# Performance work log

Hardware: AMD Instinct MI355X
Metric: run time of the kernel (lower is better)

## Reference

```python
import jax, jax.numpy as jnp
import numpy as np

EPS = 1e-5


def _binary_act(x):
    # Forward: sign(x). Backward: piecewise-polynomial surrogate (ApproxSign STE).
    out3 = jnp.where(x < -1, -1.0,
            jnp.where(x < 0, x * x + 2.0 * x,
             jnp.where(x < 1, -x * x + 2.0 * x, 1.0)))
    return jax.lax.stop_gradient(jnp.sign(x) - out3) + out3


def _binarize_weights(w):
    # Per-output-channel scaling factor (detached), forward = scale*sign(w),
    # backward flows through clamp(w, -1, 1) (STE).
    scale = jax.lax.stop_gradient(jnp.mean(jnp.abs(w), axis=(1, 2, 3), keepdims=True))
    clipped = jnp.clip(w, -1.0, 1.0)
    return jax.lax.stop_gradient(scale * jnp.sign(w) - clipped) + clipped


def setup_inputs() -> dict:
    key = jax.random.key(0)
    kx, kw = jax.random.split(key)
    B, Cin, Cout, H, W = 32, 128, 128, 56, 56
    x = jax.random.normal(kx, (B, Cin, H, W), dtype=jnp.float32)
    # HardBinaryConv: weight = rand(n)*0.001 permuted then reshaped -> just random in [0, 0.001)
    w = jax.random.uniform(kw, (Cout, Cin, 3, 3), dtype=jnp.float32) * 0.001
    return {
        "x": x,
        "bias0": jnp.zeros((Cin,), jnp.float32),   # move0 LearnableBias
        "w": w,                                     # HardBinaryConv latent weights
        "gamma": jnp.ones((Cout,), jnp.float32),    # BN weight
        "beta": jnp.zeros((Cout,), jnp.float32),    # BN bias
        "bias1": jnp.zeros((Cout,), jnp.float32),   # move1
        "alpha": jnp.full((Cout,), 0.25, jnp.float32),  # PReLU per-channel
        "bias2": jnp.zeros((Cout,), jnp.float32),   # move2
    }


def reference(x, bias0, w, gamma, beta, bias1, alpha, bias2):
    def pc(v):  # per-channel broadcast (1, C, 1, 1)
        return v[None, :, None, None]

    residual = x
    out = x + pc(bias0)                     # move0
    out = _binary_act(out)                  # binary activation
    bw = _binarize_weights(w)               # {-scale, +scale} weights
    y = jax.lax.conv_general_dilated(
        out, bw, window_strides=(1, 1), padding=((1, 1), (1, 1)),
        dimension_numbers=("NCHW", "OIHW", "NCHW"))
    # BatchNorm2d (training mode: biased batch statistics over N,H,W)
    mean = jnp.mean(y, axis=(0, 2, 3), keepdims=True)
    var = jnp.mean(jnp.square(y - mean), axis=(0, 2, 3), keepdims=True)
    y = (y - mean) * jax.lax.rsqrt(var + EPS) * pc(gamma) + pc(beta)
    y = y + residual
    y = y + pc(bias1)                       # move1
    y = jnp.where(y >= 0, y, pc(alpha) * y)  # PReLU
    y = y + pc(bias2)                       # move2
    return y
```

## Files before the change

### kernel.cpp

```cpp
#include <hip/hip_runtime.h>
#include <stdint.h>

#define NB 32
#define NC 128
#define NH 56
#define NW 56
#define NHW_ (NH * NW)
#define NPIX (NB * NHW_)
#define NO 128
#define NK 1152
#define NRP 28
#define NSLOT (NB * NRP)

#define PADH 58
#define PADW 66
#define PAD_BYTES ((size_t)NB * PADH * PADW * 2 * 8)

typedef unsigned long long u64;

__device__ __forceinline__ int wave_sum_dpp(int v) {
    v += __builtin_amdgcn_update_dpp(0, v, 0x111, 0xF, 0xF, true);
    v += __builtin_amdgcn_update_dpp(0, v, 0x112, 0xF, 0xF, true);
    v += __builtin_amdgcn_update_dpp(0, v, 0x114, 0xF, 0xF, true);
    v += __builtin_amdgcn_update_dpp(0, v, 0x118, 0xF, 0xF, true);
    v += __builtin_amdgcn_update_dpp(0, v, 0x142, 0xF, 0xF, true);
    v += __builtin_amdgcn_update_dpp(0, v, 0x143, 0xF, 0xF, true);
    return v;
}

__global__ __launch_bounds__(256) void pack_act(const float* __restrict__ x,
                                                const float* __restrict__ bias0,
                                                u64* __restrict__ packAp) {
    int p = blockIdx.x * 256 + threadIdx.x;
    if (p >= NPIX) return;
    int n = p / NHW_;
    int rem = p - n * NHW_;
    int h = rem / NW, wcol = rem - h * NW;
    const float* xb = x + (size_t)n * NC * NHW_ + rem;
    u64 w0 = 0, w1 = 0;
#pragma unroll 8
    for (int c = 0; c < 64; ++c)
        w0 |= (u64)((xb[(size_t)c * NHW_] + bias0[c]) > 0.f) << c;
#pragma unroll 8
    for (int c = 0; c < 64; ++c)
        w1 |= (u64)((xb[(size_t)(c + 64) * NHW_] + bias0[c + 64]) > 0.f) << c;
    size_t idx = (((size_t)n * PADH + (h + 1)) * PADW + (wcol + 1)) * 2;
    packAp[idx]     = w0;
    packAp[idx + 1] = w1;
}

__global__ __launch_bounds__(64) void pack_wgt(const float* __restrict__ w,
                                               u64* __restrict__ packWT,
                                               float* __restrict__ scaleW,
                                               int* __restrict__ corrW) {
    __shared__ u64 sb[18];
    int o = blockIdx.x;
    int t = threadIdx.x;
    const float* wo = w + (size_t)o * NK;
    float s = 0.f;
    for (int i = t; i < NK; i += 64) s += fabsf(wo[i]);
    for (int off = 32; off; off >>= 1) s += __shfl_down(s, off);
    if (t == 0) scaleW[o] = s / (float)NK;
    if (t < 18) {
        int tap = t >> 1;
        int j   = t & 1;
        u64 bits = 0;
        for (int cc = 0; cc < 64; ++cc) {
            int c = j * 64 + cc;
            bits |= (u64)(wo[c * 9 + tap] > 0.f) << cc;
        }
        packWT[((size_t)tap * NO + o) * 2 + j] = bits;
        sb[t] = bits;
    }
    __syncthreads();
    if (t == 0) {
        int cv[9];
#pragma unroll
        for (int tap = 0; tap < 9; ++tap)
            cv[tap] = NC - 2 * (__popcll(sb[2 * tap]) + __popcll(sb[2 * tap + 1]));
        int* cw = corrW + o * 8;
        cw[0] = cv[0] + cv[3] + cv[6];
        cw[1] = cv[2] + cv[5] + cv[8];
        cw[2] = cv[0] + cv[1] + cv[2];
        cw[3] = cv[6] + cv[7] + cv[8];
        cw[4] = cv[0];
        cw[5] = cv[2];
        cw[6] = cv[6];
        cw[7] = cv[8];
    }
}

template <int MODE>
__global__ __launch_bounds__(256) void conv_bin(
    const u64* __restrict__ packAp, const u64* __restrict__ packWT,
    const int* __restrict__ corrW, short* __restrict__ yI,
    int* __restrict__ sumP, int* __restrict__ sqP,
    const float* __restrict__ coefA, const float* __restrict__ coefB,
    const float* __restrict__ alpha, const float* __restrict__ bias2,
    const float* __restrict__ x, float* __restrict__ out) {
    __shared__ u64 lsA[4 * PADW * 2];

    int bid = blockIdx.x;
    int n = bid / (NRP * 2);
    int rem = bid - n * (NRP * 2);
    int hp = rem >> 1;
    int cg = rem & 1;
    int h0 = hp * 2;

    {
        const u64* src = packAp + ((size_t)n * PADH + h0) * PADW * 2;
        for (int i = threadIdx.x; i < 4 * PADW; i += 256) {
            ulonglong2 q = *reinterpret_cast<const ulonglong2*>(src + (size_t)i * 2);
            lsA[i * 2]     = q.x;
            lsA[i * 2 + 1] = q.y;
        }
    }
    __syncthreads();

    int wv = threadIdx.x >> 6, lane = threadIdx.x & 63;
    bool act = lane < NW;
    int obase = __builtin_amdgcn_readfirstlane(cg * 64 + (wv << 4));
    const int* cbase = corrW + obase * 8;
    const u64* lrow = lsA + (size_t)lane * 2;

    int pc0[16], pc1[16];
#pragma unroll
    for (int i = 0; i < 16; ++i) { pc0[i] = 0; pc1[i] = 0; }

#pragma unroll 1
    for (int t = 0; t < 9; ++t) {
        int kh = (t * 11) >> 5;
        int kw = t - kh * 3;
        const u64* wt = packWT + ((size_t)t * NO + obase) * 2;
        int aoff = (kh * PADW + kw) * 2;
        u64 A00 = lrow[aoff],            A01 = lrow[aoff + 1];
        u64 A10 = lrow[aoff + PADW * 2], A11 = lrow[aoff + PADW * 2 + 1];
#pragma unroll
        for (int ch = 0; ch < 16; ++ch) {
            u64 w0 = wt[2 * ch], w1 = wt[2 * ch + 1];
            pc0[ch] += __popcll(A00 ^ w0) + __popcll(A01 ^ w1);
            pc1[ch] += __popcll(A10 ^ w0) + __popcll(A11 ^ w1);
        }
    }

    bool top = (hp == 0), bot = (hp == NRP - 1);
    bool isL = (lane == 0), isR = (lane == NW - 1);
    int sl = n * NRP + hp;
    size_t pixoff = (size_t)n * NO * NHW_ + (size_t)h0 * NW + lane;

#pragma unroll
    for (int ch = 0; ch < 16; ++ch) {
        int o = obase + ch;
        const int* cw = cbase + ch * 8;
        int corrcol = isL ? cw[0] : (isR ? cw[1] : 0);
        int base = NK - corrcol;
        int d0 = base - 2 * pc0[ch];
        int d1 = base - 2 * pc1[ch];
        if (top) d0 -= cw[2] - (isL ? cw[4] : (isR ? cw[5] : 0));
        if (bot) d1 -= cw[3] - (isL ? cw[6] : (isR ? cw[7] : 0));

        if (MODE == 0 && act) {
            short* yp = yI + pixoff + (size_t)o * NHW_;
            yp[0]  = (short)d0;
            yp[NW] = (short)d1;
        }
        if (MODE <= 1) {
            int s = wave_sum_dpp(act ? (d0 + d1) : 0);
            int q = wave_sum_dpp(act ? (__mul24(d0, d0) + __mul24(d1, d1)) : 0);
            if (lane == 63) {
                sumP[o * NSLOT + sl] = s;
                sqP[o * NSLOT + sl]  = q;
            }
        }
        if (MODE == 2 && act) {
            float ca = coefA[o], cb = coefB[o], al = alpha[o], b2 = bias2[o];
            size_t idx = pixoff + (size_t)o * NHW_;
            float t0 = fmaf(ca, (float)d0, cb) + x[idx];
            float t1 = fmaf(ca, (float)d1, cb) + x[idx + NW];
            t0 = t0 >= 0.f ? t0 : al * t0;
            t1 = t1 >= 0.f ? t1 : al * t1;
            out[idx]      = t0 + b2;
            out[idx + NW] = t1 + b2;
        }
    }
}

__global__ __launch_bounds__(64) void bn_coef2(const int* __restrict__ sumP,
                                               const int* __restrict__ sqP,
                                               const float* __restrict__ scaleW,
                                               const float* __restrict__ gamma,
                                               const float* __restrict__ beta,
                                               const float* __restrict__ bias1,
                                               float* __restrict__ coefA,
                                               float* __restrict__ coefB) {
    int o = blockIdx.x;
    int t = threadIdx.x;
    long long s = 0, q = 0;
    for (int i = t; i < NSLOT; i += 64) {
        s += sumP[o * NSLOT + i];
        q += sqP[o * NSLOT + i];
    }
#pragma unroll
    for (int off = 32; off; off >>= 1) {
        s += __shfl_down(s, off);
        q += __shfl_down(q, off);
    }
    if (t == 0) {
        double cnt = (double)NPIX;
        double mean = (double)s / cnt;
        double var = (double)q / cnt - mean * mean;
        if (var < 0.0) var = 0.0;
        float sc = scaleW[o];
        float rs = rsqrtf((float)((double)sc * (double)sc * var) + 1e-5f);
        float g = gamma[o];
        coefA[o] = sc * g * rs;
        coefB[o] = beta[o] - (float)((double)sc * mean) * g * rs + bias1[o];
    }
}

__global__ __launch_bounds__(256) void final_store(const short* __restrict__ yI,
                                                   const float* __restrict__ x,
                                                   const float* __restrict__ coefA,
                                                   const float* __restrict__ coefB,
                                                   const float* __restrict__ alpha,
                                                   const float* __restrict__ bias2,
                                                   float* __restrict__ out) {
    const size_t ngroups = (size_t)NB * NO * NHW_ / 8;
    for (size_t g = (size_t)blockIdx.x * blockDim.x + threadIdx.x; g < ngroups;
         g += (size_t)gridDim.x * blockDim.x) {
        size_t i = g * 8;
        int o = (int)((i / NHW_) % NO);
        float a = coefA[o], bb = coefB[o], al = alpha[o], b2 = bias2[o];
        int4 yv = *reinterpret_cast<const int4*>(yI + i);
        float4 x0 = *reinterpret_cast<const float4*>(x + i);
        float4 x1 = *reinterpret_cast<const float4*>(x + i + 4);
        int q[4] = {yv.x, yv.y, yv.z, yv.w};
        float xs[8] = {x0.x, x0.y, x0.z, x0.w, x1.x, x1.y, x1.z, x1.w};
        float r[8];
#pragma unroll
        for (int j = 0; j < 4; ++j) {
            float lo = (float)(short)(q[j] & 0xffff);
            float hi = (float)(q[j] >> 16);
            float t0 = fmaf(a, lo, bb) + xs[2 * j];
            float t1 = fmaf(a, hi, bb) + xs[2 * j + 1];
            t0 = t0 >= 0.f ? t0 : al * t0;
            t1 = t1 >= 0.f ? t1 : al * t1;
            r[2 * j]     = t0 + b2;
            r[2 * j + 1] = t1 + b2;
        }
        float4 o0 = {r[0], r[1], r[2], r[3]};
        float4 o1 = {r[4], r[5], r[6], r[7]};
        *reinterpret_cast<float4*>(out + i)     = o0;
        *reinterpret_cast<float4*>(out + i + 4) = o1;
    }
}

extern "C" void kernel_launch(void* const* d_in, const int* in_sizes, int n_in,
                              void* d_out, int out_size, void* d_ws, size_t ws_size,
                              hipStream_t stream) {
    (void)in_sizes; (void)n_in; (void)out_size;
    const float* x     = (const float*)d_in[0];
    const float* bias0 = (const float*)d_in[1];
    const float* w     = (const float*)d_in[2];
    const float* gamma = (const float*)d_in[3];
    const float* beta  = (const float*)d_in[4];
    const float* bias1 = (const float*)d_in[5];
    const float* alpha = (const float*)d_in[6];
    const float* bias2 = (const float*)d_in[7];
    float* out = (float*)d_out;
    char* ws = (char*)d_ws;

    u64*   packAp = (u64*)ws;
    u64*   packWT = (u64*)(ws + 1959936);
    int*   corrW  = (int*)(ws + 1978368);
    float* scaleW = (float*)(ws + 1982464);
    float* coefA  = (float*)(ws + 1982976);
    float* coefB  = (float*)(ws + 1983488);
    int*   sumP   = (int*)(ws + 1984000);
    int*   sqP    = (int*)(ws + 2442752);
    short* yI     = (short*)(ws + 2901504);
    bool store = ws_size >= (size_t)2901504 + (size_t)NB * NO * NHW_ * 2;

    hipMemsetAsync(packAp, 0, PAD_BYTES, stream);
    pack_act<<<NPIX / 256, 256, 0, stream>>>(x, bias0, packAp);
    pack_wgt<<<NO, 64, 0, stream>>>(w, packWT, scaleW, corrW);

    if (store) {
        conv_bin<0><<<NB * NRP * 2, 256, 0, stream>>>(
            packAp, packWT, corrW, yI, sumP, sqP,
            nullptr, nullptr, nullptr, nullptr, nullptr, nullptr);
        bn_coef2<<<NO, 64, 0, stream>>>(sumP, sqP, scaleW, gamma, beta, bias1, coefA, coefB);
        final_store<<<2048, 256, 0, stream>>>(yI, x, coefA, coefB, alpha, bias2, out);
    } else {
        conv_bin<1><<<NB * NRP * 2, 256, 0, stream>>>(
            packAp, packWT, corrW, nullptr, sumP, sqP,
            nullptr, nullptr, nullptr, nullptr, nullptr, nullptr);
        bn_coef2<<<NO, 64, 0, stream>>>(sumP, sqP, scaleW, gamma, beta, bias1, coefA, coefB);
        conv_bin<2><<<NB * NRP * 2, 256, 0, stream>>>(
            packAp, packWT, corrW, nullptr, sumP, sqP,
            coefA, coefB, alpha, bias2, x, out);
    }
}
```

Before: 102.2 us.

## Replace XNOR-popcount binary conv with int8 MFMA implicit GEMM, recompute conv

Activations and weights are now packed as ±1 int8 values in NHWC with zero padding. The convolution runs as an implicit GEMM on 32x32x32 int8 MFMA instructions, reading from a swizzled LDS tile of six padded rows. Zero-padding the activations removes the old border-correction terms. The int16 intermediate buffer and final_store pass are dropped in favour of running the conv twice, once for the BN statistics and once fused with the epilogue, which trades double compute for less memory traffic. The int8 activation buffer is 8x larger than the bit-packed one, so packing and the memset move more bytes.

```diff
diff --git a/kernel.cpp b/kernel.cpp
--- a/kernel.cpp
+++ b/kernel.cpp
@@ -2,185 +2,203 @@
 #include <stdint.h>
 
 #define NB 32
-#define NC 128
+#define NCH 128
 #define NH 56
 #define NW 56
-#define NHW_ (NH * NW)
-#define NPIX (NB * NHW_)
-#define NO 128
-#define NK 1152
-#define NRP 28
-#define NSLOT (NB * NRP)
-
-#define PADH 58
-#define PADW 66
-#define PAD_BYTES ((size_t)NB * PADH * PADW * 2 * 8)
-
-typedef unsigned long long u64;
-
-__device__ __forceinline__ int wave_sum_dpp(int v) {
+#define NHW_ 3136
+#define NPIX 100352
+#define PADD 58
+#define IMG_BYTES ((size_t)PADD * PADD * NCH)
+#define ACT_BYTES ((size_t)NB * IMG_BYTES)
+#define NTILE 25
+#define NSLOT (NB * NTILE)
+
+typedef int v4i __attribute__((ext_vector_type(4)));
+typedef int v16i __attribute__((ext_vector_type(16)));
+
+__device__ __forceinline__ int sum32(int v) {
     v += __builtin_amdgcn_update_dpp(0, v, 0x111, 0xF, 0xF, true);
     v += __builtin_amdgcn_update_dpp(0, v, 0x112, 0xF, 0xF, true);
     v += __builtin_amdgcn_update_dpp(0, v, 0x114, 0xF, 0xF, true);
     v += __builtin_amdgcn_update_dpp(0, v, 0x118, 0xF, 0xF, true);
     v += __builtin_amdgcn_update_dpp(0, v, 0x142, 0xF, 0xF, true);
-    v += __builtin_amdgcn_update_dpp(0, v, 0x143, 0xF, 0xF, true);
     return v;
 }
 
-__global__ __launch_bounds__(256) void pack_act(const float* __restrict__ x,
-                                                const float* __restrict__ bias0,
-                                                u64* __restrict__ packAp) {
+__global__ __launch_bounds__(256) void pack_act8(const float* __restrict__ x,
+                                                 const float* __restrict__ bias0,
+                                                 char* __restrict__ act8) {
     int p = blockIdx.x * 256 + threadIdx.x;
     if (p >= NPIX) return;
     int n = p / NHW_;
     int rem = p - n * NHW_;
-    int h = rem / NW, wcol = rem - h * NW;
-    const float* xb = x + (size_t)n * NC * NHW_ + rem;
-    u64 w0 = 0, w1 = 0;
-#pragma unroll 8
-    for (int c = 0; c < 64; ++c)
-        w0 |= (u64)((xb[(size_t)c * NHW_] + bias0[c]) > 0.f) << c;
-#pragma unroll 8
-    for (int c = 0; c < 64; ++c)
-        w1 |= (u64)((xb[(size_t)(c + 64) * NHW_] + bias0[c + 64]) > 0.f) << c;
-    size_t idx = (((size_t)n * PADH + (h + 1)) * PADW + (wcol + 1)) * 2;
-    packAp[idx]     = w0;
-    packAp[idx + 1] = w1;
-}
-
-__global__ __launch_bounds__(64) void pack_wgt(const float* __restrict__ w,
-                                               u64* __restrict__ packWT,
-                                               float* __restrict__ scaleW,
-                                               int* __restrict__ corrW) {
-    __shared__ u64 sb[18];
-    int o = blockIdx.x;
-    int t = threadIdx.x;
-    const float* wo = w + (size_t)o * NK;
+    int h = rem / NW, wc = rem - (rem / NW) * NW;
+    const float* xb = x + (size_t)n * NCH * NHW_ + rem;
+    char* dst = act8 + (size_t)n * IMG_BYTES + ((size_t)(h + 1) * PADD + (wc + 1)) * NCH;
+#pragma unroll
+    for (int g = 0; g < 8; ++g) {
+        int d[4];
+#pragma unroll
+        for (int dw = 0; dw < 4; ++dw) {
+            unsigned v = 0;
+#pragma unroll
+            for (int b = 0; b < 4; ++b) {
+                int c = g * 16 + dw * 4 + b;
+                bool pos = (xb[(size_t)c * NHW_] + bias0[c]) > 0.f;
+                v |= (unsigned)(pos ? 0x01u : 0xFFu) << (8 * b);
+            }
+            d[dw] = (int)v;
+        }
+        v4i q = {d[0], d[1], d[2], d[3]};
+        *reinterpret_cast<v4i*>(dst + g * 16) = q;
+    }
+}
+
+__global__ __launch_bounds__(128) void pack_wgt8(const float* __restrict__ w,
+                                                 char* __restrict__ w8,
+                                                 float* __restrict__ scaleW) {
+    __shared__ float red[128];
+    int o = blockIdx.x, c = threadIdx.x;
+    const float* wo = w + ((size_t)o * NCH + c) * 9;
     float s = 0.f;
-    for (int i = t; i < NK; i += 64) s += fabsf(wo[i]);
-    for (int off = 32; off; off >>= 1) s += __shfl_down(s, off);
-    if (t == 0) scaleW[o] = s / (float)NK;
-    if (t < 18) {
-        int tap = t >> 1;
-        int j   = t & 1;
-        u64 bits = 0;
-        for (int cc = 0; cc < 64; ++cc) {
-            int c = j * 64 + cc;
-            bits |= (u64)(wo[c * 9 + tap] > 0.f) << cc;
-        }
-        packWT[((size_t)tap * NO + o) * 2 + j] = bits;
-        sb[t] = bits;
-    }
+#pragma unroll
+    for (int t = 0; t < 9; ++t) {
+        float v = wo[t];
+        s += fabsf(v);
+        w8[(size_t)t * NCH * NCH + (size_t)o * NCH + c] = (v > 0.f) ? 1 : -1;
+    }
+    red[c] = s;
     __syncthreads();
-    if (t == 0) {
-        int cv[9];
-#pragma unroll
-        for (int tap = 0; tap < 9; ++tap)
-            cv[tap] = NC - 2 * (__popcll(sb[2 * tap]) + __popcll(sb[2 * tap + 1]));
-        int* cw = corrW + o * 8;
-        cw[0] = cv[0] + cv[3] + cv[6];
-        cw[1] = cv[2] + cv[5] + cv[8];
-        cw[2] = cv[0] + cv[1] + cv[2];
-        cw[3] = cv[6] + cv[7] + cv[8];
-        cw[4] = cv[0];
-        cw[5] = cv[2];
-        cw[6] = cv[6];
-        cw[7] = cv[8];
-    }
+    for (int st = 64; st; st >>= 1) {
+        if (c < st) red[c] += red[c + st];
+        __syncthreads();
+    }
+    if (c == 0) scaleW[o] = red[0] / 1152.0f;
 }
 
 template <int MODE>
-__global__ __launch_bounds__(256) void conv_bin(
-    const u64* __restrict__ packAp, const u64* __restrict__ packWT,
-    const int* __restrict__ corrW, short* __restrict__ yI,
+__global__ __launch_bounds__(256) void conv_mfma(
+    const char* __restrict__ act8, const char* __restrict__ w8,
     int* __restrict__ sumP, int* __restrict__ sqP,
     const float* __restrict__ coefA, const float* __restrict__ coefB,
     const float* __restrict__ alpha, const float* __restrict__ bias2,
     const float* __restrict__ x, float* __restrict__ out) {
-    __shared__ u64 lsA[4 * PADW * 2];
+    __shared__ char lds[6 * PADD * NCH];
 
     int bid = blockIdx.x;
-    int n = bid / (NRP * 2);
-    int rem = bid - n * (NRP * 2);
-    int hp = rem >> 1;
-    int cg = rem & 1;
-    int h0 = hp * 2;
-
-    {
-        const u64* src = packAp + ((size_t)n * PADH + h0) * PADW * 2;
-        for (int i = threadIdx.x; i < 4 * PADW; i += 256) {
-            ulonglong2 q = *reinterpret_cast<const ulonglong2*>(src + (size_t)i * 2);
-            lsA[i * 2]     = q.x;
-            lsA[i * 2 + 1] = q.y;
+    int n = bid / NTILE, bt = bid - n * NTILE;
+    int pbase = bt * 128;
+    int h0 = pbase / NW;
+    bool v23 = (pbase + 64) < NHW_;
+
+    const char* an = act8 + (size_t)n * IMG_BYTES;
+    for (int r = 0; r < 6; ++r) {
+        int rp = h0 + r;
+        if (rp > 57) rp = 57;
+        const char* src = an + (size_t)rp * PADD * NCH;
+        char* drow = lds + (size_t)r * PADD * NCH;
+        for (int j = threadIdx.x; j < PADD * 8; j += 256) {
+            int col = j >> 3, g = j & 7;
+            v4i v = *reinterpret_cast<const v4i*>(src + col * NCH + g * 16);
+            *reinterpret_cast<v4i*>(drow + col * NCH + ((g ^ (col & 7)) << 4)) = v;
         }
     }
     __syncthreads();
 
     int wv = threadIdx.x >> 6, lane = threadIdx.x & 63;
-    bool act = lane < NW;
-    int obase = __builtin_amdgcn_readfirstlane(cg * 64 + (wv << 4));
-    const int* cbase = corrW + obase * 8;
-    const u64* lrow = lsA + (size_t)lane * 2;
-
-    int pc0[16], pc1[16];
-#pragma unroll
-    for (int i = 0; i < 16; ++i) { pc0[i] = 0; pc1[i] = 0; }
-
-#pragma unroll 1
-    for (int t = 0; t < 9; ++t) {
-        int kh = (t * 11) >> 5;
-        int kw = t - kh * 3;
-        const u64* wt = packWT + ((size_t)t * NO + obase) * 2;
-        int aoff = (kh * PADW + kw) * 2;
-        u64 A00 = lrow[aoff],            A01 = lrow[aoff + 1];
-        u64 A10 = lrow[aoff + PADW * 2], A11 = lrow[aoff + PADW * 2 + 1];
-#pragma unroll
-        for (int ch = 0; ch < 16; ++ch) {
-            u64 w0 = wt[2 * ch], w1 = wt[2 * ch + 1];
-            pc0[ch] += __popcll(A00 ^ w0) + __popcll(A01 ^ w1);
-            pc1[ch] += __popcll(A10 ^ w0) + __popcll(A11 ^ w1);
-        }
-    }
-
-    bool top = (hp == 0), bot = (hp == NRP - 1);
-    bool isL = (lane == 0), isR = (lane == NW - 1);
-    int sl = n * NRP + hp;
-    size_t pixoff = (size_t)n * NO * NHW_ + (size_t)h0 * NW + lane;
-
-#pragma unroll
-    for (int ch = 0; ch < 16; ++ch) {
-        int o = obase + ch;
-        const int* cw = cbase + ch * 8;
-        int corrcol = isL ? cw[0] : (isR ? cw[1] : 0);
-        int base = NK - corrcol;
-        int d0 = base - 2 * pc0[ch];
-        int d1 = base - 2 * pc1[ch];
-        if (top) d0 -= cw[2] - (isL ? cw[4] : (isR ? cw[5] : 0));
-        if (bot) d1 -= cw[3] - (isL ? cw[6] : (isR ? cw[7] : 0));
-
-        if (MODE == 0 && act) {
-            short* yp = yI + pixoff + (size_t)o * NHW_;
-            yp[0]  = (short)d0;
-            yp[NW] = (short)d1;
-        }
-        if (MODE <= 1) {
-            int s = wave_sum_dpp(act ? (d0 + d1) : 0);
-            int q = wave_sum_dpp(act ? (__mul24(d0, d0) + __mul24(d1, d1)) : 0);
-            if (lane == 63) {
-                sumP[o * NSLOT + sl] = s;
-                sqP[o * NSLOT + sl]  = q;
-            }
-        }
-        if (MODE == 2 && act) {
-            float ca = coefA[o], cb = coefB[o], al = alpha[o], b2 = bias2[o];
-            size_t idx = pixoff + (size_t)o * NHW_;
-            float t0 = fmaf(ca, (float)d0, cb) + x[idx];
-            float t1 = fmaf(ca, (float)d1, cb) + x[idx + NW];
+    int l31 = lane & 31, hl = lane >> 5;
+    int og = wv;
+
+    int p0 = pbase + l31;
+    int ph0 = p0 / NW, pw0 = p0 - ph0 * NW;
+    int p1 = p0 + 32, ph1 = p1 / NW, pw1 = p1 - ph1 * NW;
+    int p2 = p0 + 64, ph2 = p2 / NW, pw2 = p2 - ph2 * NW;
+    int p3 = p0 + 96, ph3 = p3 / NW, pw3 = p3 - ph3 * NW;
+    int rb0 = (ph0 - h0) * (PADD * NCH);
+    int rb1 = (ph1 - h0) * (PADD * NCH);
+    int rb2 = (ph2 - h0) * (PADD * NCH);
+    int rb3 = (ph3 - h0) * (PADD * NCH);
+
+    const char* wlane = w8 + ((size_t)(og * 32 + l31)) * NCH + hl * 16;
+
+    v16i acc0 = {0}, acc1 = {0}, acc2 = {0}, acc3 = {0};
+
+#pragma unroll
+    for (int tap = 0; tap < 9; ++tap) {
+        const int th = tap / 3, tw = tap - 3 * (tap / 3);
+#pragma unroll
+        for (int ks = 0; ks < 4; ++ks) {
+            v4i a = *reinterpret_cast<const v4i*>(wlane + tap * (NCH * NCH) + ks * 32);
+            int gq = ks * 2 + hl;
+            {
+                int col = pw0 + tw;
+                int off = rb0 + th * (PADD * NCH) + col * NCH + ((gq ^ (col & 7)) << 4);
+                v4i b = *reinterpret_cast<const v4i*>(lds + off);
+                acc0 = __builtin_amdgcn_mfma_i32_32x32x32_i8(a, b, acc0, 0, 0, 0);
+            }
+            {
+                int col = pw1 + tw;
+                int off = rb1 + th * (PADD * NCH) + col * NCH + ((gq ^ (col & 7)) << 4);
+                v4i b = *reinterpret_cast<const v4i*>(lds + off);
+                acc1 = __builtin_amdgcn_mfma_i32_32x32x32_i8(a, b, acc1, 0, 0, 0);
+            }
+            if (v23) {
+                {
+                    int col = pw2 + tw;
+                    int off = rb2 + th * (PADD * NCH) + col * NCH + ((gq ^ (col & 7)) << 4);
+                    v4i b = *reinterpret_cast<const v4i*>(lds + off);
+                    acc2 = __builtin_amdgcn_mfma_i32_32x32x32_i8(a, b, acc2, 0, 0, 0);
+                }
+                {
+                    int col = pw3 + tw;
+                    int off = rb3 + th * (PADD * NCH) + col * NCH + ((gq ^ (col & 7)) << 4);
+                    v4i b = *reinterpret_cast<const v4i*>(lds + off);
+                    acc3 = __builtin_amdgcn_mfma_i32_32x32x32_i8(a, b, acc3, 0, 0, 0);
+                }
+            }
+        }
+    }
+
+    if (MODE == 0) {
+        int slot = n * NTILE + bt;
+#pragma unroll
+        for (int r = 0; r < 16; ++r) {
+            int d0 = acc0[r], d1 = acc1[r];
+            int s = d0 + d1;
+            int q = d0 * d0 + d1 * d1;
+            if (v23) {
+                int d2 = acc2[r], d3 = acc3[r];
+                s += d2 + d3;
+                q += d2 * d2 + d3 * d3;
+            }
+            s = sum32(s);
+            q = sum32(q);
+            if (l31 == 31) {
+                int ch = og * 32 + (r & 3) + 8 * (r >> 2) + 4 * hl;
+                sumP[ch * NSLOT + slot] = s;
+                sqP[ch * NSLOT + slot] = q;
+            }
+        }
+    } else {
+#pragma unroll
+        for (int r = 0; r < 16; ++r) {
+            int ch = og * 32 + (r & 3) + 8 * (r >> 2) + 4 * hl;
+            float ca = coefA[ch], cb = coefB[ch], al = alpha[ch], b2 = bias2[ch];
+            size_t base = ((size_t)n * NCH + ch) * NHW_ + pbase + l31;
+            float t0 = fmaf(ca, (float)acc0[r], cb) + x[base];
             t0 = t0 >= 0.f ? t0 : al * t0;
+            out[base] = t0 + b2;
+            float t1 = fmaf(ca, (float)acc1[r], cb) + x[base + 32];
             t1 = t1 >= 0.f ? t1 : al * t1;
-            out[idx]      = t0 + b2;
-            out[idx + NW] = t1 + b2;
+            out[base + 32] = t1 + b2;
+            if (v23) {
+                float t2 = fmaf(ca, (float)acc2[r], cb) + x[base + 64];
+                t2 = t2 >= 0.f ? t2 : al * t2;
+                out[base + 64] = t2 + b2;
+                float t3 = fmaf(ca, (float)acc3[r], cb) + x[base + 96];
+                t3 = t3 >= 0.f ? t3 : al * t3;
+                out[base + 96] = t3 + b2;
+            }
         }
     }
 }
@@ -218,47 +236,10 @@
     }
 }
 
-__global__ __launch_bounds__(256) void final_store(const short* __restrict__ yI,
-                                                   const float* __restrict__ x,
-                                                   const float* __restrict__ coefA,
-                                                   const float* __restrict__ coefB,
-                                                   const float* __restrict__ alpha,
-                                                   const float* __restrict__ bias2,
-                                                   float* __restrict__ out) {
-    const size_t ngroups = (size_t)NB * NO * NHW_ / 8;
-    for (size_t g = (size_t)blockIdx.x * blockDim.x + threadIdx.x; g < ngroups;
-         g += (size_t)gridDim.x * blockDim.x) {
-        size_t i = g * 8;
-        int o = (int)((i / NHW_) % NO);
-        float a = coefA[o], bb = coefB[o], al = alpha[o], b2 = bias2[o];
-        int4 yv = *reinterpret_cast<const int4*>(yI + i);
-        float4 x0 = *reinterpret_cast<const float4*>(x + i);
-        float4 x1 = *reinterpret_cast<const float4*>(x + i + 4);
-        int q[4] = {yv.x, yv.y, yv.z, yv.w};
-        float xs[8] = {x0.x, x0.y, x0.z, x0.w, x1.x, x1.y, x1.z, x1.w};
-        float r[8];
-#pragma unroll
-        for (int j = 0; j < 4; ++j) {
-            float lo = (float)(short)(q[j] & 0xffff);
-            float hi = (float)(q[j] >> 16);
-            float t0 = fmaf(a, lo, bb) + xs[2 * j];
-            float t1 = fmaf(a, hi, bb) + xs[2 * j + 1];
-            t0 = t0 >= 0.f ? t0 : al * t0;
-            t1 = t1 >= 0.f ? t1 : al * t1;
-            r[2 * j]     = t0 + b2;
-            r[2 * j + 1] = t1 + b2;
-        }
-        float4 o0 = {r[0], r[1], r[2], r[3]};
-        float4 o1 = {r[4], r[5], r[6], r[7]};
-        *reinterpret_cast<float4*>(out + i)     = o0;
-        *reinterpret_cast<float4*>(out + i + 4) = o1;
-    }
-}
-
 extern "C" void kernel_launch(void* const* d_in, const int* in_sizes, int n_in,
                               void* d_out, int out_size, void* d_ws, size_t ws_size,
                               hipStream_t stream) {
-    (void)in_sizes; (void)n_in; (void)out_size;
+    (void)in_sizes; (void)n_in; (void)out_size; (void)ws_size;
     const float* x     = (const float*)d_in[0];
     const float* bias0 = (const float*)d_in[1];
     const float* w     = (const float*)d_in[2];
@@ -270,34 +251,21 @@
     float* out = (float*)d_out;
     char* ws = (char*)d_ws;
 
-    u64*   packAp = (u64*)ws;
-    u64*   packWT = (u64*)(ws + 1959936);
-    int*   corrW  = (int*)(ws + 1978368);
-    float* scaleW = (float*)(ws + 1982464);
-    float* coefA  = (float*)(ws + 1982976);
-    float* coefB  = (float*)(ws + 1983488);
-    int*   sumP   = (int*)(ws + 1984000);
-    int*   sqP    = (int*)(ws + 2442752);
-    short* yI     = (short*)(ws + 2901504);
-    bool store = ws_size >= (size_t)2901504 + (size_t)NB * NO * NHW_ * 2;
-
-    hipMemsetAsync(packAp, 0, PAD_BYTES, stream);
-    pack_act<<<NPIX / 256, 256, 0, stream>>>(x, bias0, packAp);
-    pack_wgt<<<NO, 64, 0, stream>>>(w, packWT, scaleW, corrW);
-
-    if (store) {
-        conv_bin<0><<<NB * NRP * 2, 256, 0, stream>>>(
-            packAp, packWT, corrW, yI, sumP, sqP,
-            nullptr, nullptr, nullptr, nullptr, nullptr, nullptr);
-        bn_coef2<<<NO, 64, 0, stream>>>(sumP, sqP, scaleW, gamma, beta, bias1, coefA, coefB);
-        final_store<<<2048, 256, 0, stream>>>(yI, x, coefA, coefB, alpha, bias2, out);
-    } else {
-        conv_bin<1><<<NB * NRP * 2, 256, 0, stream>>>(
-            packAp, packWT, corrW, nullptr, sumP, sqP,
-            nullptr, nullptr, nullptr, nullptr, nullptr, nullptr);
-        bn_coef2<<<NO, 64, 0, stream>>>(sumP, sqP, scaleW, gamma, beta, bias1, coefA, coefB);
-        conv_bin<2><<<NB * NRP * 2, 256, 0, stream>>>(
-            packAp, packWT, corrW, nullptr, sumP, sqP,
-            coefA, coefB, alpha, bias2, x, out);
-    }
-}
+    char*  act8   = ws;
+    char*  w8     = ws + 13778944;
+    float* scaleW = (float*)(ws + 13926400);
+    float* coefA  = (float*)(ws + 13926912);
+    float* coefB  = (float*)(ws + 13927424);
+    int*   sumP   = (int*)(ws + 13927936);
+    int*   sqP    = (int*)(ws + 14337536);
+
+    hipMemsetAsync(act8, 0, ACT_BYTES, stream);
+    pack_act8<<<(NPIX + 255) / 256, 256, 0, stream>>>(x, bias0, act8);
+    pack_wgt8<<<NCH, 128, 0, stream>>>(w, w8, scaleW);
+
+    conv_mfma<0><<<NB * NTILE, 256, 0, stream>>>(
+        act8, w8, sumP, sqP, nullptr, nullptr, nullptr, nullptr, nullptr, nullptr);
+    bn_coef2<<<NCH, 64, 0, stream>>>(sumP, sqP, scaleW, gamma, beta, bias1, coefA, coefB);
+    conv_mfma<1><<<NB * NTILE, 256, 0, stream>>>(
+        act8, w8, sumP, sqP, coefA, coefB, alpha, bias2, x, out);
+}
```

Result: slower. 117.1 us (+14.5%).
